# Kernel tuning notes

Measured on AMD Instinct MI355X. Metric: run time of the kernel, lower is better.

## Reference

```python
import jax, jax.numpy as jnp
import numpy as np

B, T, C, L = 256, 512, 128, 64  # batch, timesteps, num_classes (blank=C-1), max label len
NEG = -1e30  # finite -inf surrogate (avoids nan in grads)


def setup_inputs() -> dict:
    key = jax.random.key(0)
    k1, k2, k3, k4 = jax.random.split(key, 4)
    logits = jax.random.normal(k1, (B, T, C), dtype=jnp.float32)
    y_pred = jax.nn.softmax(logits, axis=-1)  # ctc_batch_cost expects softmax probs
    y_true = jax.random.randint(k2, (B, L), 0, C - 1, dtype=jnp.int32)  # non-blank labels
    input_length = jax.random.randint(k3, (B, 1), T // 2, T + 1, dtype=jnp.int32)
    label_length = jax.random.randint(k4, (B, 1), L // 2, L + 1, dtype=jnp.int32)
    return {"y_true": y_true, "y_pred": y_pred,
            "input_length": input_length, "label_length": label_length}


def _ctc_loss(log_probs, labels, input_length, label_length, blank):
    # log_probs: [B,T,C]; labels: [B,L]; lengths: [B]
    b, t_max, _ = log_probs.shape
    l_max = labels.shape[1]
    s_max = 2 * l_max + 1
    # extended label sequence: blank, l1, blank, l2, ..., blank  -> [B,S]
    ext = jnp.full((b, s_max), blank, dtype=labels.dtype)
    ext = ext.at[:, 1::2].set(labels)
    # gathered log probs per extended symbol: [B,T,S]
    lp = jnp.take_along_axis(log_probs, ext[:, None, :].astype(jnp.int32), axis=2)
    # skip (s-2 -> s) allowed where ext[s] != blank and ext[s] != ext[s-2]
    skip = jnp.zeros((b, s_max), dtype=bool)
    skip = skip.at[:, 2:].set((ext[:, 2:] != blank) & (ext[:, 2:] != ext[:, :-2]))
    # init alpha at t=0: only s=0 (blank) and s=1 (first label) reachable
    alpha0 = jnp.full((b, s_max), NEG, dtype=log_probs.dtype)
    alpha0 = alpha0.at[:, 0].set(lp[:, 0, 0])
    alpha0 = alpha0.at[:, 1].set(lp[:, 0, 1])
    in_len = input_length

    def step(alpha, inp):
        lp_t, t = inp  # lp_t: [B,S]
        s1 = jnp.pad(alpha, ((0, 0), (1, 0)), constant_values=NEG)[:, :-1]
        s2 = jnp.pad(alpha, ((0, 0), (2, 0)), constant_values=NEG)[:, :-2]
        a = jnp.logaddexp(alpha, s1)
        a = jnp.where(skip, jnp.logaddexp(a, s2), a)
        new = a + lp_t
        new = jnp.where((t < in_len)[:, None], new, alpha)  # freeze past input_length
        return new, None

    lp_time_major = jnp.swapaxes(lp, 0, 1)  # [T,B,S]
    ts = jnp.arange(1, t_max)
    alpha, _ = jax.lax.scan(step, alpha0, (lp_time_major[1:], ts))
    lab = label_length
    idx_last = 2 * lab  # final blank position; idx_last-1 is final label position
    a_last = jnp.take_along_axis(alpha, idx_last[:, None], axis=1)[:, 0]
    a_prev = jnp.take_along_axis(alpha, (idx_last - 1)[:, None], axis=1)[:, 0]
    return -jnp.logaddexp(a_last, a_prev)  # [B]


def reference(y_true, y_pred, input_length, label_length):
    eps = 1e-7  # keras epsilon added before log
    log_probs = jnp.log(y_pred + eps)
    blank = y_pred.shape[-1] - 1  # keras ctc_batch_cost blank convention
    loss = _ctc_loss(log_probs, y_true, input_length[:, 0], label_length[:, 0], blank)
    return loss[:, None]  # [B,1], matching tf expand_dims(ctc_loss, 1)
```

## Files before the change

### kernel.cpp

```cpp
#include <hip/hip_runtime.h>


#define B_ 256
#define T_ 512
#define C_ 128
#define L_ 64
#define BLANK_ 127
#define EPSF (1e-7f)
#define CHUNK 32
#define QSTR 36
#define LN2F 0.6931471805599453f

#define EXP2(x) __builtin_amdgcn_exp2f(x)
#define LOG2(x) __builtin_amdgcn_logf(x)

__device__ __forceinline__ float lse2_2(float a, float b) {
    float m = fmaxf(a, b);
    float d = fminf(a, b) - m;
    return m + LOG2(1.0f + EXP2(d));
}

__device__ __forceinline__ float dppf(float x) {
    return __int_as_float(__builtin_amdgcn_update_dpp(
        0, __float_as_int(x), 0x138, 0xf, 0xf, false));
}
__device__ __forceinline__ int dppi(int x) {
    return __builtin_amdgcn_update_dpp(0, x, 0x138, 0xf, 0xf, false);
}

__device__ __forceinline__ float delta_scale(int ep, int e) {
    int d = ep - e;
    d = d < -126 ? -126 : d;
    d = d > 126 ? 126 : d;
    return __int_as_float((d + 127) << 23);
}

__device__ __forceinline__ void renorm(float& A0, float& A1, float& A2, int& e) {
    const float m = fmaxf(fmaxf(A0, A1), A2);
    const int ex = (__float_as_int(m) >> 23) - 127;
    const float s = __int_as_float((127 - ex) << 23);
    A0 *= s; A1 *= s; A2 *= s;
    e += ex;
}

__device__ __forceinline__ void stage_chunk(const float* gsrc, float* ldst, int lane) {
#pragma unroll
    for (int i = 0; i < CHUNK / 2; ++i) {
        __builtin_amdgcn_global_load_lds(
            (const __attribute__((address_space(1))) void*)(gsrc + i * 256 + lane * 4),
            (__attribute__((address_space(3))) void*)(ldst + i * 256),
            16, 0, 0);
    }
}

__device__ __forceinline__ void produce_chunk(const float* __restrict__ rk,
        float* __restrict__ qd, int lane, int label, int t0, int tend, float& llg)
{
    const float pbv  = rk[(lane & 31) * C_ + BLANK_] + EPSF;
    const float rpb  = 1.0f / pbv;
    const float erpb = EPSF * rpb;
    const int t = t0 + lane;
    const bool lgv = (lane < 32) && (t >= 1) && (t < tend);
    llg += lgv ? LOG2(pbv) : 0.0f;
#pragma unroll
    for (int r = 0; r < CHUNK; ++r) {
        const float pl = rk[r * C_ + label];
        const float rb = __int_as_float(
            __builtin_amdgcn_readlane(__float_as_int(rpb), r));
        const float eb = __int_as_float(
            __builtin_amdgcn_readlane(__float_as_int(erpb), r));
        qd[lane * QSTR + r] = fmaf(pl, rb, eb);
    }
}

__device__ __forceinline__ void fat_step(float& A0, float& A1, float& A2, int& e,
                                         float skipf, float ql) {
    const float p1 = dppf(A1);
    const int   ep = dppi(e);
    const bool dead = (A0 + A1) == 0.0f;
    const int   e1 = dead ? ep : e;
    const float P1 = p1 * delta_scale(ep, e1);
    const float A0o = A0, A1o = A1;
    A0 = A0o + P1;
    const float t = fmaf(skipf, P1, A0o);
    A1 = (A1o + t) * ql;
    A2 = A2 + A1o;
    e  = e1;
}

__device__ __forceinline__ void lean_step(float& A0, float& A1, float& A2,
                                          float sc, float skipf, float ql) {
    const float P1 = dppf(A1) * sc;
    const float A0o = A0, A1o = A1;
    A0 = A0o + P1;
    const float t = fmaf(skipf, P1, A0o);
    A1 = (A1o + t) * ql;
    A2 = A2 + A1o;
}

__global__ __launch_bounds__(128) void ctc_fwd_kernel(
    const int* __restrict__ y_true, const float* __restrict__ y_pred,
    const int* __restrict__ input_len, const int* __restrict__ label_len,
    float* __restrict__ out)
{
    __shared__ __align__(16) float raw[2][CHUNK * C_];
    __shared__ __align__(16) float qlbuf[2][64 * QSTR];
    __shared__ float extra[4];

    const int b = blockIdx.x;
    const int tid = threadIdx.x;
    const int lane = tid & 63;
    const float* __restrict__ Pg = y_pred + (size_t)b * T_ * C_;
    const int label = y_true[b * L_ + lane];
    const int in_len = input_len[b];
    const int tend = in_len < T_ ? in_len : T_;
    const int nmax = (tend + CHUNK - 1) / CHUNK;

    if (tid >= 64) {
        float llg = 0.0f;
        stage_chunk(Pg, &raw[0][0], lane);
        stage_chunk(Pg + CHUNK * C_, &raw[1][0], lane);
        asm volatile("s_waitcnt vmcnt(16)" ::: "memory");
        produce_chunk(&raw[0][0], &qlbuf[0][0], lane, label, 0, tend, llg);
        if (lane == 0) {
            extra[0] = raw[0][label] + EPSF;
            extra[1] = raw[0][BLANK_] + EPSF;
        }
        asm volatile("s_waitcnt lgkmcnt(0)" ::: "memory");
        __builtin_amdgcn_s_barrier();
        for (int c = 0; c < nmax; ++c) {
            if (c + 2 < nmax)
                stage_chunk(Pg + (size_t)(c + 2) * CHUNK * C_, &raw[c & 1][0], lane);
            if (c + 1 < nmax) {
                if (c + 2 < nmax) asm volatile("s_waitcnt vmcnt(16)" ::: "memory");
                else              asm volatile("s_waitcnt vmcnt(0)" ::: "memory");
                produce_chunk(&raw[(c + 1) & 1][0], &qlbuf[(c + 1) & 1][0],
                              lane, label, (c + 1) * CHUNK, tend, llg);
            }
            asm volatile("s_waitcnt lgkmcnt(0)" ::: "memory");
            __builtin_amdgcn_s_barrier();
        }
#pragma unroll
        for (int off = 16; off >= 1; off >>= 1) llg += __shfl_xor(llg, off);
        if (lane == 0) extra[2] = llg;
        asm volatile("s_waitcnt lgkmcnt(0)" ::: "memory");
        __builtin_amdgcn_s_barrier();
    } else {
        const int lprev = __shfl_up(label, 1);
        const float skipf = (lane > 0 && label != lprev) ? 1.0f : 0.0f;
        const int lab = label_len[b];
        __builtin_amdgcn_s_barrier();

        float A0 = (lane == 0) ? extra[1] : 0.0f;
        float A1 = (lane == 0) ? extra[0] : 0.0f;
        float A2 = 0.0f, sc = 1.0f;
        int e = 0;

        {
            const float* qb = &qlbuf[0][lane * QSTR];
            float qlv[32];
#pragma unroll
            for (int k = 0; k < 8; ++k) {
                const float4 t4 = *reinterpret_cast<const float4*>(qb + 4 * k);
                qlv[4*k+0] = t4.x; qlv[4*k+1] = t4.y;
                qlv[4*k+2] = t4.z; qlv[4*k+3] = t4.w;
            }
            __builtin_amdgcn_sched_barrier(0);
#pragma unroll
            for (int u = 1; u < 32; ++u) {
                fat_step(A0, A1, A2, e, skipf, qlv[u]);
                if ((u & 3) == 3) renorm(A0, A1, A2, e);
            }
            __builtin_amdgcn_s_barrier();
        }
        for (int c = 1; c < 4; ++c) {
            const float* qb = &qlbuf[c & 1][lane * QSTR];
            float qlv[32];
#pragma unroll
            for (int k = 0; k < 8; ++k) {
                const float4 t4 = *reinterpret_cast<const float4*>(qb + 4 * k);
                qlv[4*k+0] = t4.x; qlv[4*k+1] = t4.y;
                qlv[4*k+2] = t4.z; qlv[4*k+3] = t4.w;
            }
            __builtin_amdgcn_sched_barrier(0);
#pragma unroll
            for (int u = 0; u < 32; ++u) {
                fat_step(A0, A1, A2, e, skipf, qlv[u]);
                if ((u & 3) == 3) renorm(A0, A1, A2, e);
            }
            __builtin_amdgcn_s_barrier();
        }
        sc = delta_scale(dppi(e), e);
        for (int c = 4; c < nmax; ++c) {
            const float* qb = &qlbuf[c & 1][lane * QSTR];
            float qlv[32];
#pragma unroll
            for (int k = 0; k < 8; ++k) {
                const float4 t4 = *reinterpret_cast<const float4*>(qb + 4 * k);
                qlv[4*k+0] = t4.x; qlv[4*k+1] = t4.y;
                qlv[4*k+2] = t4.z; qlv[4*k+3] = t4.w;
            }
            __builtin_amdgcn_sched_barrier(0);
            const int rem = tend - c * CHUNK;
            if (rem >= CHUNK) {
#pragma unroll
                for (int u = 0; u < 32; ++u) {
                    lean_step(A0, A1, A2, sc, skipf, qlv[u]);
                    if ((u & 3) == 3) {
                        renorm(A0, A1, A2, e);
                        sc = delta_scale(dppi(e), e);
                    }
                }
            } else {
#pragma unroll
                for (int u = 0; u < 32; ++u) {
                    const float A0o = A0, A1o = A1, A2o = A2;
                    lean_step(A0, A1, A2, sc, skipf, qlv[u]);
                    const bool v = u < rem;
                    A0 = v ? A0 : A0o; A1 = v ? A1 : A1o; A2 = v ? A2 : A2o;
                    if ((u & 3) == 3) {
                        renorm(A0, A1, A2, e);
                        sc = delta_scale(dppi(e), e);
                    }
                }
            }
            __builtin_amdgcn_s_barrier();
        }
        __builtin_amdgcn_s_barrier();
        const float lg = extra[2];
        const float ef = (float)e + lg;
        const float l0 = LOG2(A0) + ef;
        const float l1 = LOG2(A1) + ef;
        const float l2 = LOG2(A2) + ef;
        const float a_prev = __shfl(l1, lab - 1);
        const float a_last = (lab >= L_) ? __shfl(l2, 63)
                                         : __shfl(l0, lab);
        if (lane == 0) out[b] = -LN2F * lse2_2(a_last, a_prev);
    }
}

extern "C" void kernel_launch(void* const* d_in, const int* in_sizes, int n_in,
                              void* d_out, int out_size, void* d_ws, size_t ws_size,
                              hipStream_t stream) {
    const int*   y_true    = (const int*)d_in[0];
    const float* y_pred    = (const float*)d_in[1];
    const int*   input_len = (const int*)d_in[2];
    const int*   label_len = (const int*)d_in[3];
    float* out = (float*)d_out;

    ctc_fwd_kernel<<<B_, 128, 0, stream>>>(y_true, y_pred, input_len, label_len, out);
}
```

Measured before the change: 26.07 us.

## Use lazy ballot-gated renormalization with half-scaled recurrence and templated consumer

Replaces the unconditional per-4-step exponent renormalization with a wave-wide check that rescales only when any lane's magnitude leaves a safe range. Folds a factor of 0.5 into each step so values stay bounded, and compensates with a (tend-1) log2 term at the end. Specializes the consumer on whether the label length equals 64 to drop the A2 track when unused. It also vectorizes the LDS stores in the producer and stops the tail loop at the remaining step count. The per-step critical path gets shorter, at the cost of a wave ballot branch and some risk of precision drift between rescales.

New measurement: 24.33 us. 6.7% less time.

```diff
diff --git a/kernel.cpp b/kernel.cpp
--- a/kernel.cpp
+++ b/kernel.cpp
@@ -28,21 +28,6 @@
     return __builtin_amdgcn_update_dpp(0, x, 0x138, 0xf, 0xf, false);
 }
 
-__device__ __forceinline__ float delta_scale(int ep, int e) {
-    int d = ep - e;
-    d = d < -126 ? -126 : d;
-    d = d > 126 ? 126 : d;
-    return __int_as_float((d + 127) << 23);
-}
-
-__device__ __forceinline__ void renorm(float& A0, float& A1, float& A2, int& e) {
-    const float m = fmaxf(fmaxf(A0, A1), A2);
-    const int ex = (__float_as_int(m) >> 23) - 127;
-    const float s = __int_as_float((127 - ex) << 23);
-    A0 *= s; A1 *= s; A2 *= s;
-    e += ex;
-}
-
 __device__ __forceinline__ void stage_chunk(const float* gsrc, float* ldst, int lane) {
 #pragma unroll
     for (int i = 0; i < CHUNK / 2; ++i) {
@@ -57,45 +42,122 @@
         float* __restrict__ qd, int lane, int label, int t0, int tend, float& llg)
 {
     const float pbv  = rk[(lane & 31) * C_ + BLANK_] + EPSF;
-    const float rpb  = 1.0f / pbv;
+    const float rpb  = 0.5f / pbv;
     const float erpb = EPSF * rpb;
     const int t = t0 + lane;
     const bool lgv = (lane < 32) && (t >= 1) && (t < tend);
     llg += lgv ? LOG2(pbv) : 0.0f;
 #pragma unroll
-    for (int r = 0; r < CHUNK; ++r) {
-        const float pl = rk[r * C_ + label];
-        const float rb = __int_as_float(
-            __builtin_amdgcn_readlane(__float_as_int(rpb), r));
-        const float eb = __int_as_float(
-            __builtin_amdgcn_readlane(__float_as_int(erpb), r));
-        qd[lane * QSTR + r] = fmaf(pl, rb, eb);
-    }
-}
-
-__device__ __forceinline__ void fat_step(float& A0, float& A1, float& A2, int& e,
-                                         float skipf, float ql) {
-    const float p1 = dppf(A1);
-    const int   ep = dppi(e);
-    const bool dead = (A0 + A1) == 0.0f;
-    const int   e1 = dead ? ep : e;
-    const float P1 = p1 * delta_scale(ep, e1);
+    for (int k = 0; k < 8; ++k) {
+        float q[4];
+#pragma unroll
+        for (int j = 0; j < 4; ++j) {
+            const int r = 4 * k + j;
+            const float pl = rk[r * C_ + label];
+            const float rb = __int_as_float(
+                __builtin_amdgcn_readlane(__float_as_int(rpb), r));
+            const float eb = __int_as_float(
+                __builtin_amdgcn_readlane(__float_as_int(erpb), r));
+            q[j] = fmaf(pl, rb, eb);
+        }
+        *reinterpret_cast<float4*>(qd + lane * QSTR + 4 * k) =
+            make_float4(q[0], q[1], q[2], q[3]);
+    }
+}
+
+template<bool HAS128>
+__device__ __forceinline__ void maybe_renorm(float& A0, float& A1, float& A2,
+                                             int& e, float& sch) {
+    float m2 = fmaxf(A0, A1);
+    if (HAS128) m2 = fmaxf(m2, A2);
+    const bool out = (m2 > 16777216.0f) ||
+                     ((m2 < 5.9604644775390625e-8f) && (m2 > 0.0f));
+    if (__any(out)) {
+        const float mm = (m2 == 0.0f) ? 1.0f : m2;
+        const int eb = __float_as_int(mm) >> 23;
+        const float s = __int_as_float((254 - eb) << 23);
+        A0 *= s; A1 *= s;
+        if (HAS128) A2 *= s;
+        e += eb - 127;
+        const int ep = dppi(e);
+        int d = ep - e;
+        d = d < -125 ? -125 : d;
+        d = d > 127 ? 127 : d;
+        sch = __int_as_float((d + 126) << 23);
+    }
+}
+
+template<bool HAS128>
+__device__ __forceinline__ void step(float& A0, float& A1, float& A2,
+                                     float sch, float skipf2, float ql) {
+    const float P1 = dppf(A1) * sch;
     const float A0o = A0, A1o = A1;
-    A0 = A0o + P1;
-    const float t = fmaf(skipf, P1, A0o);
+    A0 = fmaf(A0o, 0.5f, P1);
+    const float t = fmaf(skipf2, P1, A0o);
     A1 = (A1o + t) * ql;
-    A2 = A2 + A1o;
-    e  = e1;
-}
-
-__device__ __forceinline__ void lean_step(float& A0, float& A1, float& A2,
-                                          float sc, float skipf, float ql) {
-    const float P1 = dppf(A1) * sc;
-    const float A0o = A0, A1o = A1;
-    A0 = A0o + P1;
-    const float t = fmaf(skipf, P1, A0o);
-    A1 = (A1o + t) * ql;
-    A2 = A2 + A1o;
+    if (HAS128) A2 = (A2 + A1o) * 0.5f;
+}
+
+template<bool HAS128>
+__device__ __forceinline__ void consumer(const float (*qlbuf)[64 * QSTR],
+        const float* extra, int lane, int label, int lab, int tend, int nmax,
+        float* out, int b)
+{
+    const int lprev = __shfl_up(label, 1);
+    const float skipf2 = (lane > 0 && label != lprev) ? 2.0f : 0.0f;
+
+    float A0 = 0.0f, A1 = 0.0f, A2 = 0.0f, sch = 0.5f;
+    int e = 0;
+
+    for (int c = 0; c < nmax; ++c) {
+        const float* qb = &qlbuf[c & 1][lane * QSTR];
+        float qlv[32];
+#pragma unroll
+        for (int k = 0; k < 8; ++k) {
+            const float4 t4 = *reinterpret_cast<const float4*>(qb + 4 * k);
+            qlv[4*k+0] = t4.x; qlv[4*k+1] = t4.y;
+            qlv[4*k+2] = t4.z; qlv[4*k+3] = t4.w;
+        }
+        asm volatile("s_waitcnt lgkmcnt(0)" ::: "memory");
+        __builtin_amdgcn_s_barrier();
+        __builtin_amdgcn_sched_barrier(0);
+
+        const int rem = tend - c * CHUNK;
+        if (c == 0) {
+            A0 = (lane == 0) ? extra[1] : 0.0f;
+            A1 = (lane == 0) ? extra[0] : 0.0f;
+#pragma unroll
+            for (int u = 1; u < 32; ++u) {
+                step<HAS128>(A0, A1, A2, sch, skipf2, qlv[u]);
+                if ((u & 3) == 3) maybe_renorm<HAS128>(A0, A1, A2, e, sch);
+            }
+        } else if (rem >= CHUNK) {
+#pragma unroll
+            for (int u = 0; u < 32; ++u) {
+                step<HAS128>(A0, A1, A2, sch, skipf2, qlv[u]);
+                if ((u & 3) == 3) maybe_renorm<HAS128>(A0, A1, A2, e, sch);
+            }
+        } else {
+            for (int u = 0; u < rem; ++u) {
+                step<HAS128>(A0, A1, A2, sch, skipf2, qlv[u]);
+                if ((u & 3) == 3) maybe_renorm<HAS128>(A0, A1, A2, e, sch);
+            }
+        }
+    }
+    __builtin_amdgcn_s_barrier();
+    const float lg = extra[2];
+    const float ef = (float)e + lg + (float)(tend - 1);
+    const float l0 = LOG2(A0) + ef;
+    const float l1 = LOG2(A1) + ef;
+    const float a_prev = __shfl(l1, lab - 1);
+    float a_last;
+    if (HAS128) {
+        const float l2 = LOG2(A2) + ef;
+        a_last = __shfl(l2, 63);
+    } else {
+        a_last = __shfl(l0, lab);
+    }
+    if (lane == 0) out[b] = -LN2F * lse2_2(a_last, a_prev);
 }
 
 __global__ __launch_bounds__(128) void ctc_fwd_kernel(
@@ -146,96 +208,10 @@
         asm volatile("s_waitcnt lgkmcnt(0)" ::: "memory");
         __builtin_amdgcn_s_barrier();
     } else {
-        const int lprev = __shfl_up(label, 1);
-        const float skipf = (lane > 0 && label != lprev) ? 1.0f : 0.0f;
         const int lab = label_len[b];
         __builtin_amdgcn_s_barrier();
-
-        float A0 = (lane == 0) ? extra[1] : 0.0f;
-        float A1 = (lane == 0) ? extra[0] : 0.0f;
-        float A2 = 0.0f, sc = 1.0f;
-        int e = 0;
-
-        {
-            const float* qb = &qlbuf[0][lane * QSTR];
-            float qlv[32];
-#pragma unroll
-            for (int k = 0; k < 8; ++k) {
-                const float4 t4 = *reinterpret_cast<const float4*>(qb + 4 * k);
-                qlv[4*k+0] = t4.x; qlv[4*k+1] = t4.y;
-                qlv[4*k+2] = t4.z; qlv[4*k+3] = t4.w;
-            }
-            __builtin_amdgcn_sched_barrier(0);
-#pragma unroll
-            for (int u = 1; u < 32; ++u) {
-                fat_step(A0, A1, A2, e, skipf, qlv[u]);
-                if ((u & 3) == 3) renorm(A0, A1, A2, e);
-            }
-            __builtin_amdgcn_s_barrier();
-        }
-        for (int c = 1; c < 4; ++c) {
-            const float* qb = &qlbuf[c & 1][lane * QSTR];
-            float qlv[32];
-#pragma unroll
-            for (int k = 0; k < 8; ++k) {
-                const float4 t4 = *reinterpret_cast<const float4*>(qb + 4 * k);
-                qlv[4*k+0] = t4.x; qlv[4*k+1] = t4.y;
-                qlv[4*k+2] = t4.z; qlv[4*k+3] = t4.w;
-            }
-            __builtin_amdgcn_sched_barrier(0);
-#pragma unroll
-            for (int u = 0; u < 32; ++u) {
-                fat_step(A0, A1, A2, e, skipf, qlv[u]);
-                if ((u & 3) == 3) renorm(A0, A1, A2, e);
-            }
-            __builtin_amdgcn_s_barrier();
-        }
-        sc = delta_scale(dppi(e), e);
-        for (int c = 4; c < nmax; ++c) {
-            const float* qb = &qlbuf[c & 1][lane * QSTR];
-            float qlv[32];
-#pragma unroll
-            for (int k = 0; k < 8; ++k) {
-                const float4 t4 = *reinterpret_cast<const float4*>(qb + 4 * k);
-                qlv[4*k+0] = t4.x; qlv[4*k+1] = t4.y;
-                qlv[4*k+2] = t4.z; qlv[4*k+3] = t4.w;
-            }
-            __builtin_amdgcn_sched_barrier(0);
-            const int rem = tend - c * CHUNK;
-            if (rem >= CHUNK) {
-#pragma unroll
-                for (int u = 0; u < 32; ++u) {
-                    lean_step(A0, A1, A2, sc, skipf, qlv[u]);
-                    if ((u & 3) == 3) {
-                        renorm(A0, A1, A2, e);
-                        sc = delta_scale(dppi(e), e);
-                    }
-                }
-            } else {
-#pragma unroll
-                for (int u = 0; u < 32; ++u) {
-                    const float A0o = A0, A1o = A1, A2o = A2;
-                    lean_step(A0, A1, A2, sc, skipf, qlv[u]);
-                    const bool v = u < rem;
-                    A0 = v ? A0 : A0o; A1 = v ? A1 : A1o; A2 = v ? A2 : A2o;
-                    if ((u & 3) == 3) {
-                        renorm(A0, A1, A2, e);
-                        sc = delta_scale(dppi(e), e);
-                    }
-                }
-            }
-            __builtin_amdgcn_s_barrier();
-        }
-        __builtin_amdgcn_s_barrier();
-        const float lg = extra[2];
-        const float ef = (float)e + lg;
-        const float l0 = LOG2(A0) + ef;
-        const float l1 = LOG2(A1) + ef;
-        const float l2 = LOG2(A2) + ef;
-        const float a_prev = __shfl(l1, lab - 1);
-        const float a_last = (lab >= L_) ? __shfl(l2, 63)
-                                         : __shfl(l0, lab);
-        if (lane == 0) out[b] = -LN2F * lse2_2(a_last, a_prev);
+        if (lab == L_) consumer<true >(qlbuf, extra, lane, label, lab, tend, nmax, out, b);
+        else           consumer<false>(qlbuf, extra, lane, label, lab, tend, nmax, out, b);
     }
 }
 
```
